# Kernel tuning notes

Measured on AMD Instinct MI355X. Metric: run time of the kernel, lower is better.

## Reference

```python
import jax, jax.numpy as jnp
import numpy as np

B, C, Cs, CI, H, W = 4, 256, 256, 128, 64, 64

def setup_inputs() -> dict:
    key = jax.random.key(0)
    ks = jax.random.split(key, 9)
    sq = 1.0 / np.sqrt(C)
    ss = 1.0 / np.sqrt(Cs)
    return {
        "x_main": jax.random.normal(ks[0], (B, C, H, W), jnp.float32),
        "z_p": jax.random.normal(ks[1], (B, Cs, H, W), jnp.float32),
        "Wq": jax.random.normal(ks[2], (CI, C), jnp.float32) * sq,
        "bq": jax.random.normal(ks[3], (CI,), jnp.float32) * 0.01,
        "Wk": jax.random.normal(ks[4], (CI, Cs), jnp.float32) * ss,
        "bk": jax.random.normal(ks[5], (CI,), jnp.float32) * 0.01,
        "Wv": jax.random.normal(ks[6], (C, Cs), jnp.float32) * ss,
        "bv": jax.random.normal(ks[7], (C,), jnp.float32) * 0.01,
        "gamma": jax.random.normal(ks[8], (1,), jnp.float32) * 0.1,
    }

def reference(x_main, z_p, Wq, bq, Wk, bk, Wv, bv, gamma):
    b, c, h, w = x_main.shape
    n = h * w
    xm = x_main.reshape(b, c, n)          # [B, C, N]
    zf = z_p.reshape(b, z_p.shape[1], n)  # [B, Cs, M] (M == N here)
    # 1x1 convs == per-pixel channel projections
    q = jnp.einsum('oc,bcn->bon', Wq, xm) + bq[None, :, None]  # [B, CI, N]
    k = jnp.einsum('oc,bcm->bom', Wk, zf) + bk[None, :, None]  # [B, CI, M]
    v = jnp.einsum('oc,bcm->bom', Wv, zf) + bv[None, :, None]  # [B, C, M]
    # energy[b, n, m] = q_n . k_m  (no scaling, as in the original)
    energy = jnp.einsum('bcn,bcm->bnm', q, k)
    attention = jax.nn.softmax(energy, axis=-1)
    out = jnp.einsum('bom,bnm->bon', v, attention)  # [B, C, N]
    out = out.reshape(b, c, h, w)
    return gamma * out + x_main
```

## Files before the change

kernel.cpp:

```cpp
#include <hip/hip_runtime.h>
#include <hip/hip_bf16.h>


typedef __bf16  bf16x8  __attribute__((ext_vector_type(8)));
typedef float   f32x16  __attribute__((ext_vector_type(16)));

#define LOG2E 1.4426950408889634f

union BF8 { __hip_bfloat162 h[4]; bf16x8 v; };
union U4  { unsigned u[4]; bf16x8 v; };

__device__ inline bf16x8 pack8(const float f[8]) {
  BF8 u;
#pragma unroll
  for (int i = 0; i < 4; i++)
    u.h[i] = __float22bfloat162_rn(float2{f[2 * i], f[2 * i + 1]});
  return u.v;
}

__device__ inline void dma16(const void* g, void* l) {
  __builtin_amdgcn_global_load_lds(
      (const __attribute__((address_space(1))) unsigned int*)g,
      (__attribute__((address_space(3))) unsigned int*)l, 16, 0, 0);
}

__global__ __launch_bounds__(256) void wprep_kernel(
    const float* __restrict__ Wq, const float* __restrict__ Wk,
    const float* __restrict__ Wv, __hip_bfloat16* __restrict__ wfr)
{
  const int base = blockIdx.x * 1024;
  const int tid = threadIdx.x;
#pragma unroll
  for (int i = 0; i < 4; i++) {
    int c = base + i * 256 + tid;
    const float* Ws; __hip_bfloat16* dst; int rc;
    if (c < 4096)      { Ws = Wq; dst = wfr;          rc = c; }
    else if (c < 8192) { Ws = Wk; dst = wfr + 32768;  rc = c - 4096; }
    else               { Ws = Wv; dst = wfr + 65536;  rc = c - 8192; }
    int ot = rc >> 10, cs = (rc >> 6) & 15, rem = rc & 63;
    int hf = rem >> 5, l32 = rem & 31;
    const float* src = Ws + (ot * 32 + l32) * 256 + cs * 16 + hf * 8;
    float f[8];
#pragma unroll
    for (int j = 0; j < 8; j++) f[j] = src[j];
    *(bf16x8*)(dst + ot * 8192 + cs * 512 + hf * 256 + l32 * 8) = pack8(f);
  }
}

struct PFSmem {
  float stg[128 * 68];
  alignas(16) __hip_bfloat16 frag[16384];
};

__global__ __launch_bounds__(512, 2) void projfused(
    const float* __restrict__ x, const float* __restrict__ z,
    const __hip_bfloat16* __restrict__ wfr,
    const float* __restrict__ bq, const float* __restrict__ bk,
    const float* __restrict__ bv,
    __hip_bfloat16* __restrict__ qp, __hip_bfloat16* __restrict__ kp,
    __hip_bfloat16* __restrict__ vp)
{
  __shared__ PFSmem sm;
  const int bi = blockIdx.x;
  const bool qmode = bi < 256;
  const int j2 = qmode ? bi : bi - 256;
  const int b = j2 >> 6, pc = j2 & 63;
  const float* in = qmode ? x : z;
  const size_t ib = (size_t)b * 256 * 4096 + pc * 64;

  const int tid = threadIdx.x, w = tid >> 6, lane = tid & 63,
            l32 = lane & 31, half = lane >> 5;
  const int pix4 = (tid & 15) * 4;

#pragma unroll
  for (int it = 0; it < 4; it++) {
    int ch = it * 32 + (tid >> 4);
    float4 v4 = *(const float4*)&in[ib + (size_t)ch * 4096 + pix4];
    *(float4*)&sm.stg[ch * 68 + pix4] = v4;
  }
  __syncthreads();
#pragma unroll
  for (int i = 0; i < 2; i++) {
    int c = i * 512 + tid;
    int grp = c >> 9, csl = (c >> 6) & 7, rem = c & 63;
    int hf = rem >> 5, lr = rem & 31;
    int chb = csl * 16 + hf * 8;
    float f[8];
#pragma unroll
    for (int j = 0; j < 8; j++) f[j] = sm.stg[(chb + j) * 68 + grp * 32 + lr];
    *(bf16x8*)(sm.frag + grp * 8192 + csl * 512 + hf * 256 + lr * 8) = pack8(f);
  }
  __syncthreads();

#pragma unroll
  for (int it = 0; it < 4; it++) {
    int ch = it * 32 + (tid >> 4);
    float4 v4 = *(const float4*)&in[ib + (size_t)(128 + ch) * 4096 + pix4];
    *(float4*)&sm.stg[ch * 68 + pix4] = v4;
  }
  __syncthreads();
#pragma unroll
  for (int i = 0; i < 2; i++) {
    int c = i * 512 + tid;
    int grp = c >> 9, csl = (c >> 6) & 7, rem = c & 63;
    int hf = rem >> 5, lr = rem & 31;
    int chb = csl * 16 + hf * 8;
    float f[8];
#pragma unroll
    for (int j = 0; j < 8; j++) f[j] = sm.stg[(chb + j) * 68 + grp * 32 + lr];
    *(bf16x8*)(sm.frag + grp * 8192 + (csl + 8) * 512 + hf * 256 + lr * 8) =
        pack8(f);
  }
  __syncthreads();

  const int t4 = (l32 >> 2) & 3;
  const int kperm = (t4 == 1 || t4 == 2) ? (l32 ^ 12) : l32;

  if (qmode) {
    const int ot = w >> 1, pg = w & 1;
    bf16x8 bfr[16];
#pragma unroll
    for (int cs = 0; cs < 16; cs++)
      bfr[cs] = *(const bf16x8*)(sm.frag + pg * 8192 + cs * 512 + lane * 8);
    const __hip_bfloat16* wp = wfr + ot * 8192 + lane * 8;
    bf16x8 wfg[16];
#pragma unroll
    for (int cs = 0; cs < 16; cs++) wfg[cs] = *(const bf16x8*)(wp + cs * 512);
    float bb[16];
#pragma unroll
    for (int r = 0; r < 16; r++)
      bb[r] = bq[ot * 32 + (r & 3) + 8 * (r >> 2) + 4 * half];
    f32x16 O = {};
#pragma unroll
    for (int cs = 0; cs < 16; cs++)
      O = __builtin_amdgcn_mfma_f32_32x32x16_bf16(wfg[cs], bfr[cs], O, 0, 0, 0);
    __hip_bfloat16* qb = qp + ((size_t)(b * 128 + pc * 2 + pg)) * 4096;
#pragma unroll
    for (int r = 0; r < 16; r++) {
      int oc = ot * 32 + (r & 3) + 8 * (r >> 2) + 4 * half;
      qb[(oc >> 4) * 512 + ((oc >> 3) & 1) * 256 + l32 * 8 + (oc & 7)] =
          __float2bfloat16((O[r] + bb[r]) * LOG2E);
    }
  } else {
    const int pg = w & 1;
    bf16x8 bfr[16];
#pragma unroll
    for (int cs = 0; cs < 16; cs++)
      bfr[cs] = *(const bf16x8*)(sm.frag + pg * 8192 + cs * 512 + lane * 8);
    const size_t pgg = (size_t)(b * 128 + pc * 2 + pg);
#pragma unroll
    for (int jj = 0; jj < 3; jj++) {
      const int t = (w + jj * 8) >> 1;
      const bool isK = (t < 4);
      const __hip_bfloat16* wp = wfr + (isK ? 32768 + t * 8192
                                            : 65536 + (t - 4) * 8192) + lane * 8;
      bf16x8 wfg[16];
#pragma unroll
      for (int cs = 0; cs < 16; cs++) wfg[cs] = *(const bf16x8*)(wp + cs * 512);
      const float* bias = isK ? bk : bv;
      const int ocb = (isK ? t : t - 4) * 32;
      float bb[16];
#pragma unroll
      for (int r = 0; r < 16; r++)
        bb[r] = bias[ocb + (r & 3) + 8 * (r >> 2) + 4 * half];
      f32x16 O = {};
#pragma unroll
      for (int cs = 0; cs < 16; cs++)
        O = __builtin_amdgcn_mfma_f32_32x32x16_bf16(wfg[cs], bfr[cs], O, 0, 0, 0);
      if (isK) {
        __hip_bfloat16* kb = kp + pgg * 4096;
#pragma unroll
        for (int r = 0; r < 16; r++) {
          int oc = t * 32 + (r & 3) + 8 * (r >> 2) + 4 * half;
          kb[(oc >> 4) * 512 + ((oc >> 3) & 1) * 256 + kperm * 8 + (oc & 7)] =
              __float2bfloat16(O[r] + bb[r]);
        }
      } else {
        __hip_bfloat16* vb = vp + pgg * 8192 + (t - 4) * 1024
            + (l32 >> 4) * 512 + ((l32 >> 3) & 1) * 256 + (l32 & 7);
#pragma unroll
        for (int r = 0; r < 16; r++) {
          int rr = (r & 3) + 8 * (r >> 2) + 4 * half;
          vb[rr * 8] = __float2bfloat16(O[r] + bb[r]);
        }
      }
    }
  }
}

struct AttnSmem {
  union {
    __hip_bfloat16 kbuf[3][8192];
    float ostage[256][33];
  } u;
  float redu[4][32];
  float rinv[32];
};

__global__ __launch_bounds__(256, 3) void attn_kernel(
    const __hip_bfloat16* __restrict__ qv, const __hip_bfloat16* __restrict__ kv,
    const __hip_bfloat16* __restrict__ vv,
    const float* __restrict__ x_main, const float* __restrict__ gammap,
    float* __restrict__ out)
{
  __shared__ AttnSmem sm;
  const int i  = blockIdx.x;
  const int b  = (i & 7) >> 1;
  const int qt = ((i >> 3) << 1) | (i & 1);
  const int n0 = qt * 32;
  const int tid  = threadIdx.x;
  const int w    = tid >> 6, lane = tid & 63, l32 = lane & 31;
  const int kh   = w >> 1, chh = w & 1;
  const int t0   = qt & 63;

  bf16x8 qf[8];
  {
    const __hip_bfloat16* qb = qv + ((size_t)(b * 128 + qt)) * 4096 + lane * 8;
#pragma unroll
    for (int cs = 0; cs < 8; cs++) qf[cs] = *(const bf16x8*)(qb + cs * 512);
  }

  const __hip_bfloat16* kg = kv + (size_t)(b * 128) * 4096;
  const __hip_bfloat16* vg = vv + (size_t)(b * 128) * 8192;

  auto stage = [&](int ta, int par) {
    __hip_bfloat16* kd = sm.u.kbuf[par];
    const __hip_bfloat16* ksrc = kg + (size_t)ta * 8192 + lane * 8;
#pragma unroll
    for (int c = 0; c < 4; c++) {
      int ck = w * 4 + c;
      dma16(ksrc + ck * 512, kd + ck * 512 + lane * 8);
    }
  };

  f32x16 Oacc[4];
#pragma unroll
  for (int c = 0; c < 4; c++)
#pragma unroll
    for (int r = 0; r < 16; r++) Oacc[c][r] = 0.f;

  float l_lane = 0.f;

  stage(t0, 0);
  stage((t0 + 1) & 63, 1);
  __syncthreads();

#pragma unroll 1
  for (int lt = 0; lt < 64; ++lt) {
    const int ta = (lt + t0) & 63;

    const __hip_bfloat16* vb = vg + (size_t)(ta * 2 + kh) * 8192
                             + chh * 4096 + lane * 8;
    bf16x8 Vc[8];
#pragma unroll
    for (int c = 0; c < 4; c++) {
      Vc[2 * c]     = *(const bf16x8*)(vb + c * 1024);
      Vc[2 * c + 1] = *(const bf16x8*)(vb + c * 1024 + 512);
    }
    __builtin_amdgcn_sched_barrier(0);

    if (lt < 62) stage((lt + 2 + t0) & 63, (lt + 2) % 3);

    const __hip_bfloat16* kbase = sm.u.kbuf[lt % 3] + kh * 4096 + lane * 8;
    f32x16 S = {};
#pragma unroll
    for (int cs = 0; cs < 8; cs++) {
      bf16x8 kf = *(const bf16x8*)(kbase + cs * 512);
      S = __builtin_amdgcn_mfma_f32_32x32x16_bf16(kf, qf[cs], S, 0, 0, 0);
    }

    unsigned p2[8];
    float lsub = 0.f;
#pragma unroll
    for (int i2 = 0; i2 < 8; i2++) {
      float a = exp2f(S[2 * i2]     - 64.0f);
      float c = exp2f(S[2 * i2 + 1] - 64.0f);
      lsub += a + c;
      union { __hip_bfloat162 h; unsigned u; } cv;
      cv.h = __float22bfloat162_rn(float2{a, c});
      p2[i2] = cv.u;
    }
    l_lane += lsub;
    U4 f0, f1;
    f0.u[0] = p2[0]; f0.u[1] = p2[1]; f0.u[2] = p2[2]; f0.u[3] = p2[3];
    f1.u[0] = p2[4]; f1.u[1] = p2[5]; f1.u[2] = p2[6]; f1.u[3] = p2[7];
    const bf16x8 pf0 = f0.v, pf1 = f1.v;

#pragma unroll
    for (int c = 0; c < 4; c++) {
      Oacc[c] = __builtin_amdgcn_mfma_f32_32x32x16_bf16(Vc[2 * c],     pf0, Oacc[c], 0, 0, 0);
      Oacc[c] = __builtin_amdgcn_mfma_f32_32x32x16_bf16(Vc[2 * c + 1], pf1, Oacc[c], 0, 0, 0);
    }

    if (lt < 63) {
      __builtin_amdgcn_sched_barrier(0);
      __builtin_amdgcn_s_barrier();
      __builtin_amdgcn_sched_barrier(0);
    }
  }

  float lfull = l_lane + __shfl_xor(l_lane, 32);
  if (lane < 32) sm.redu[w][l32] = lfull;
  __syncthreads();
  const int hb = lane >> 5;
  if (kh == 0) {
#pragma unroll
    for (int c = 0; c < 4; c++) {
#pragma unroll
      for (int r = 0; r < 16; r++) {
        int ch = (chh * 4 + c) * 32 + (r & 3) + 8 * (r >> 2) + 4 * hb;
        sm.u.ostage[ch][l32] = Oacc[c][r];
      }
    }
  }
  if (tid < 32) sm.rinv[tid] = 1.0f / (sm.redu[0][tid] + sm.redu[2][tid]);
  __syncthreads();
  if (kh == 1) {
#pragma unroll
    for (int c = 0; c < 4; c++) {
#pragma unroll
      for (int r = 0; r < 16; r++) {
        int ch = (chh * 4 + c) * 32 + (r & 3) + 8 * (r >> 2) + 4 * hb;
        sm.u.ostage[ch][l32] += Oacc[c][r];
      }
    }
  }
  __syncthreads();

  const float gmm = gammap[0];
  const int pix = tid & 31;
  const float ri = sm.rinv[pix];
#pragma unroll
  for (int j = 0; j < 32; ++j) {
    int ch = (tid >> 5) * 32 + j;
    size_t g = ((size_t)(b * 256 + ch)) * 4096 + n0 + pix;
    out[g] = gmm * sm.u.ostage[ch][pix] * ri + x_main[g];
  }
}

extern "C" void kernel_launch(void* const* d_in, const int* in_sizes, int n_in,
                              void* d_out, int out_size, void* d_ws, size_t ws_size,
                              hipStream_t stream) {
  (void)in_sizes; (void)n_in; (void)out_size; (void)ws_size;
  const float* x  = (const float*)d_in[0];
  const float* z  = (const float*)d_in[1];
  const float* Wq = (const float*)d_in[2];
  const float* bq = (const float*)d_in[3];
  const float* Wk = (const float*)d_in[4];
  const float* bk = (const float*)d_in[5];
  const float* Wv = (const float*)d_in[6];
  const float* bv = (const float*)d_in[7];
  const float* gm = (const float*)d_in[8];
  float* out = (float*)d_out;

  char* ws = (char*)d_ws;
  const size_t MB = 1024 * 1024;
  __hip_bfloat16* qp  = (__hip_bfloat16*)(ws);
  __hip_bfloat16* kp  = (__hip_bfloat16*)(ws + 4 * MB);
  __hip_bfloat16* vp  = (__hip_bfloat16*)(ws + 8 * MB);
  __hip_bfloat16* wfp = (__hip_bfloat16*)(ws + 16 * MB);

  wprep_kernel<<<16, 256, 0, stream>>>(Wq, Wk, Wv, wfp);
  projfused   <<<512, 512, 0, stream>>>(x, z, wfp, bq, bk, bv, qp, kp, vp);
  attn_kernel <<<512, 256, 0, stream>>>(qp, kp, vp, x, gm, out);
}
```

Measured before the change: 202.6 us.

## Process two query tiles per attention block to reuse K/V loads

Each attention block now handles 64 queries as two 32-query sub-tiles that share the same staged K tile and V registers, and the grid is halved to 256 blocks. Q moves into LDS, and the epilogue staging, row-sum reduction and output write are widened to 64 pixels. The aim is to halve global and LDS traffic for K and V per unit of work. In exchange, accumulator register use doubles and launch bounds drop to one block per CU, so fewer waves are left to hide latency.

```diff
diff --git a/kernel.cpp b/kernel.cpp
--- a/kernel.cpp
+++ b/kernel.cpp
@@ -190,41 +190,46 @@
 
 struct AttnSmem {
   union {
-    __hip_bfloat16 kbuf[3][8192];
-    float ostage[256][33];
+    struct {
+      __hip_bfloat16 kbuf[3][8192];
+      __hip_bfloat16 qlds[8192];
+    } m;
+    float ostage[256][65];
   } u;
-  float redu[4][32];
-  float rinv[32];
+  float redu[4][64];
+  float rinv[64];
 };
 
-__global__ __launch_bounds__(256, 3) void attn_kernel(
+__global__ __launch_bounds__(256, 1) void attn_kernel(
     const __hip_bfloat16* __restrict__ qv, const __hip_bfloat16* __restrict__ kv,
     const __hip_bfloat16* __restrict__ vv,
     const float* __restrict__ x_main, const float* __restrict__ gammap,
     float* __restrict__ out)
 {
   __shared__ AttnSmem sm;
-  const int i  = blockIdx.x;
-  const int b  = (i & 7) >> 1;
-  const int qt = ((i >> 3) << 1) | (i & 1);
-  const int n0 = qt * 32;
-  const int tid  = threadIdx.x;
-  const int w    = tid >> 6, lane = tid & 63, l32 = lane & 31;
-  const int kh   = w >> 1, chh = w & 1;
-  const int t0   = qt & 63;
-
-  bf16x8 qf[8];
+  const int i   = blockIdx.x;
+  const int b   = (i & 7) >> 1;
+  const int qt2 = ((i >> 3) << 1) | (i & 1);
+  const int qtA = qt2 * 2;
+  const int n0  = qt2 * 64;
+  const int tid = threadIdx.x;
+  const int w   = tid >> 6, lane = tid & 63, l32 = lane & 31;
+  const int kh  = w >> 1, chh = w & 1;
+  const int t0  = qt2 & 63;
+
   {
-    const __hip_bfloat16* qb = qv + ((size_t)(b * 128 + qt)) * 4096 + lane * 8;
-#pragma unroll
-    for (int cs = 0; cs < 8; cs++) qf[cs] = *(const bf16x8*)(qb + cs * 512);
+    const __hip_bfloat16* qsrc = qv + ((size_t)(b * 128 + qtA)) * 4096;
+#pragma unroll
+    for (int j = 0; j < 4; j++)
+      *(bf16x8*)(sm.u.m.qlds + j * 2048 + tid * 8) =
+          *(const bf16x8*)(qsrc + j * 2048 + tid * 8);
   }
 
   const __hip_bfloat16* kg = kv + (size_t)(b * 128) * 4096;
   const __hip_bfloat16* vg = vv + (size_t)(b * 128) * 8192;
 
   auto stage = [&](int ta, int par) {
-    __hip_bfloat16* kd = sm.u.kbuf[par];
+    __hip_bfloat16* kd = sm.u.m.kbuf[par];
     const __hip_bfloat16* ksrc = kg + (size_t)ta * 8192 + lane * 8;
 #pragma unroll
     for (int c = 0; c < 4; c++) {
@@ -233,42 +238,15 @@
     }
   };
 
-  f32x16 Oacc[4];
+  f32x16 OA[4], OB[4];
 #pragma unroll
   for (int c = 0; c < 4; c++)
 #pragma unroll
-    for (int r = 0; r < 16; r++) Oacc[c][r] = 0.f;
-
-  float l_lane = 0.f;
-
-  stage(t0, 0);
-  stage((t0 + 1) & 63, 1);
-  __syncthreads();
-
-#pragma unroll 1
-  for (int lt = 0; lt < 64; ++lt) {
-    const int ta = (lt + t0) & 63;
-
-    const __hip_bfloat16* vb = vg + (size_t)(ta * 2 + kh) * 8192
-                             + chh * 4096 + lane * 8;
-    bf16x8 Vc[8];
-#pragma unroll
-    for (int c = 0; c < 4; c++) {
-      Vc[2 * c]     = *(const bf16x8*)(vb + c * 1024);
-      Vc[2 * c + 1] = *(const bf16x8*)(vb + c * 1024 + 512);
-    }
-    __builtin_amdgcn_sched_barrier(0);
-
-    if (lt < 62) stage((lt + 2 + t0) & 63, (lt + 2) % 3);
-
-    const __hip_bfloat16* kbase = sm.u.kbuf[lt % 3] + kh * 4096 + lane * 8;
-    f32x16 S = {};
-#pragma unroll
-    for (int cs = 0; cs < 8; cs++) {
-      bf16x8 kf = *(const bf16x8*)(kbase + cs * 512);
-      S = __builtin_amdgcn_mfma_f32_32x32x16_bf16(kf, qf[cs], S, 0, 0, 0);
-    }
-
+    for (int r = 0; r < 16; r++) { OA[c][r] = 0.f; OB[c][r] = 0.f; }
+
+  float lA = 0.f, lB = 0.f;
+
+  auto softmax = [&](const f32x16& S, bf16x8& pf0, bf16x8& pf1, float& lacc) {
     unsigned p2[8];
     float lsub = 0.f;
 #pragma unroll
@@ -280,16 +258,57 @@
       cv.h = __float22bfloat162_rn(float2{a, c});
       p2[i2] = cv.u;
     }
-    l_lane += lsub;
+    lacc += lsub;
     U4 f0, f1;
     f0.u[0] = p2[0]; f0.u[1] = p2[1]; f0.u[2] = p2[2]; f0.u[3] = p2[3];
     f1.u[0] = p2[4]; f1.u[1] = p2[5]; f1.u[2] = p2[6]; f1.u[3] = p2[7];
-    const bf16x8 pf0 = f0.v, pf1 = f1.v;
-
-#pragma unroll
-    for (int c = 0; c < 4; c++) {
-      Oacc[c] = __builtin_amdgcn_mfma_f32_32x32x16_bf16(Vc[2 * c],     pf0, Oacc[c], 0, 0, 0);
-      Oacc[c] = __builtin_amdgcn_mfma_f32_32x32x16_bf16(Vc[2 * c + 1], pf1, Oacc[c], 0, 0, 0);
+    pf0 = f0.v; pf1 = f1.v;
+  };
+
+  stage(t0, 0);
+  stage((t0 + 1) & 63, 1);
+  __syncthreads();
+
+#pragma unroll 1
+  for (int lt = 0; lt < 64; ++lt) {
+    const int ta = (lt + t0) & 63;
+
+    const __hip_bfloat16* vb = vg + (size_t)(ta * 2 + kh) * 8192
+                             + chh * 4096 + lane * 8;
+    bf16x8 Vc[8];
+#pragma unroll
+    for (int c = 0; c < 4; c++) {
+      Vc[2 * c]     = *(const bf16x8*)(vb + c * 1024);
+      Vc[2 * c + 1] = *(const bf16x8*)(vb + c * 1024 + 512);
+    }
+    __builtin_amdgcn_sched_barrier(0);
+
+    if (lt < 62) stage((lt + 2 + t0) & 63, (lt + 2) % 3);
+
+    const __hip_bfloat16* kbase = sm.u.m.kbuf[lt % 3] + kh * 4096 + lane * 8;
+    const __hip_bfloat16* qab   = sm.u.m.qlds + lane * 8;
+    f32x16 SA = {}, SB = {};
+#pragma unroll
+    for (int cs = 0; cs < 8; cs++) {
+      bf16x8 kf = *(const bf16x8*)(kbase + cs * 512);
+      bf16x8 qa = *(const bf16x8*)(qab + cs * 512);
+      bf16x8 qb2 = *(const bf16x8*)(qab + 4096 + cs * 512);
+      SA = __builtin_amdgcn_mfma_f32_32x32x16_bf16(kf, qa,  SA, 0, 0, 0);
+      SB = __builtin_amdgcn_mfma_f32_32x32x16_bf16(kf, qb2, SB, 0, 0, 0);
+    }
+
+    bf16x8 pf0, pf1;
+    softmax(SA, pf0, pf1, lA);
+#pragma unroll
+    for (int c = 0; c < 4; c++) {
+      OA[c] = __builtin_amdgcn_mfma_f32_32x32x16_bf16(Vc[2 * c],     pf0, OA[c], 0, 0, 0);
+      OA[c] = __builtin_amdgcn_mfma_f32_32x32x16_bf16(Vc[2 * c + 1], pf1, OA[c], 0, 0, 0);
+    }
+    softmax(SB, pf0, pf1, lB);
+#pragma unroll
+    for (int c = 0; c < 4; c++) {
+      OB[c] = __builtin_amdgcn_mfma_f32_32x32x16_bf16(Vc[2 * c],     pf0, OB[c], 0, 0, 0);
+      OB[c] = __builtin_amdgcn_mfma_f32_32x32x16_bf16(Vc[2 * c + 1], pf1, OB[c], 0, 0, 0);
     }
 
     if (lt < 63) {
@@ -299,8 +318,9 @@
     }
   }
 
-  float lfull = l_lane + __shfl_xor(l_lane, 32);
-  if (lane < 32) sm.redu[w][l32] = lfull;
+  float lfA = lA + __shfl_xor(lA, 32);
+  float lfB = lB + __shfl_xor(lB, 32);
+  if (lane < 32) { sm.redu[w][l32] = lfA; sm.redu[w][32 + l32] = lfB; }
   __syncthreads();
   const int hb = lane >> 5;
   if (kh == 0) {
@@ -309,11 +329,12 @@
 #pragma unroll
       for (int r = 0; r < 16; r++) {
         int ch = (chh * 4 + c) * 32 + (r & 3) + 8 * (r >> 2) + 4 * hb;
-        sm.u.ostage[ch][l32] = Oacc[c][r];
+        sm.u.ostage[ch][l32]      = OA[c][r];
+        sm.u.ostage[ch][32 + l32] = OB[c][r];
       }
     }
   }
-  if (tid < 32) sm.rinv[tid] = 1.0f / (sm.redu[0][tid] + sm.redu[2][tid]);
+  if (tid < 64) sm.rinv[tid] = 1.0f / (sm.redu[0][tid] + sm.redu[2][tid]);
   __syncthreads();
   if (kh == 1) {
 #pragma unroll
@@ -321,18 +342,19 @@
 #pragma unroll
       for (int r = 0; r < 16; r++) {
         int ch = (chh * 4 + c) * 32 + (r & 3) + 8 * (r >> 2) + 4 * hb;
-        sm.u.ostage[ch][l32] += Oacc[c][r];
+        sm.u.ostage[ch][l32]      += OA[c][r];
+        sm.u.ostage[ch][32 + l32] += OB[c][r];
       }
     }
   }
   __syncthreads();
 
   const float gmm = gammap[0];
-  const int pix = tid & 31;
+  const int pix = tid & 63;
   const float ri = sm.rinv[pix];
-#pragma unroll
-  for (int j = 0; j < 32; ++j) {
-    int ch = (tid >> 5) * 32 + j;
+#pragma unroll 1
+  for (int j = 0; j < 64; ++j) {
+    int ch = j * 4 + (tid >> 6);
     size_t g = ((size_t)(b * 256 + ch)) * 4096 + n0 + pix;
     out[g] = gmm * sm.u.ostage[ch][pix] * ri + x_main[g];
   }
@@ -362,5 +384,5 @@
 
   wprep_kernel<<<16, 256, 0, stream>>>(Wq, Wk, Wv, wfp);
   projfused   <<<512, 512, 0, stream>>>(x, z, wfp, bq, bk, bv, qp, kp, vp);
-  attn_kernel <<<512, 256, 0, stream>>>(qp, kp, vp, x, gm, out);
-}
+  attn_kernel <<<256, 256, 0, stream>>>(qp, kp, vp, x, gm, out);
+}
```

New measurement: 227.3 us. +12.2%, slower.

## Split MFMA accumulation chains and stage Q/K projection outputs through LDS

Applied to the files above, without the earlier changes.

Splits each dependent MFMA accumulation chain into two independent accumulators (for the Q/K/V projections and the QK^T score product), so consecutive MFMAs do not wait on each other's results. In the projection kernel, Q and K outputs are first written into shared memory, then copied to global memory with coalesced 16-byte vector stores in place of scattered 2-byte stores. The cost is extra accumulator registers, an added barrier and LDS traffic, and slightly different floating-point summation order.

```diff
diff --git a/kernel.cpp b/kernel.cpp
--- a/kernel.cpp
+++ b/kernel.cpp
@@ -115,6 +115,7 @@
 
   const int t4 = (l32 >> 2) & 3;
   const int kperm = (t4 == 1 || t4 == 2) ? (l32 ^ 12) : l32;
+  __hip_bfloat16* ostg = (__hip_bfloat16*)sm.stg;
 
   if (qmode) {
     const int ot = w >> 1, pg = w & 1;
@@ -130,17 +131,23 @@
 #pragma unroll
     for (int r = 0; r < 16; r++)
       bb[r] = bq[ot * 32 + (r & 3) + 8 * (r >> 2) + 4 * half];
-    f32x16 O = {};
-#pragma unroll
-    for (int cs = 0; cs < 16; cs++)
-      O = __builtin_amdgcn_mfma_f32_32x32x16_bf16(wfg[cs], bfr[cs], O, 0, 0, 0);
-    __hip_bfloat16* qb = qp + ((size_t)(b * 128 + pc * 2 + pg)) * 4096;
+    f32x16 Oa = {}, Ob = {};
+#pragma unroll
+    for (int cs = 0; cs < 8; cs++) {
+      Oa = __builtin_amdgcn_mfma_f32_32x32x16_bf16(wfg[cs],     bfr[cs],     Oa, 0, 0, 0);
+      Ob = __builtin_amdgcn_mfma_f32_32x32x16_bf16(wfg[cs + 8], bfr[cs + 8], Ob, 0, 0, 0);
+    }
 #pragma unroll
     for (int r = 0; r < 16; r++) {
       int oc = ot * 32 + (r & 3) + 8 * (r >> 2) + 4 * half;
-      qb[(oc >> 4) * 512 + ((oc >> 3) & 1) * 256 + l32 * 8 + (oc & 7)] =
-          __float2bfloat16((O[r] + bb[r]) * LOG2E);
-    }
+      ostg[pg * 4096 + (oc >> 4) * 512 + ((oc >> 3) & 1) * 256 + l32 * 8 +
+           (oc & 7)] =
+          __float2bfloat16((Oa[r] + Ob[r] + bb[r]) * LOG2E);
+    }
+    __syncthreads();
+    __hip_bfloat16* qb = qp + ((size_t)(b * 128 + pc * 2)) * 4096;
+    *(bf16x8*)(qb + tid * 8)        = *(const bf16x8*)(ostg + tid * 8);
+    *(bf16x8*)(qb + 4096 + tid * 8) = *(const bf16x8*)(ostg + 4096 + tid * 8);
   } else {
     const int pg = w & 1;
     bf16x8 bfr[16];
@@ -148,41 +155,61 @@
     for (int cs = 0; cs < 16; cs++)
       bfr[cs] = *(const bf16x8*)(sm.frag + pg * 8192 + cs * 512 + lane * 8);
     const size_t pgg = (size_t)(b * 128 + pc * 2 + pg);
-#pragma unroll
-    for (int jj = 0; jj < 3; jj++) {
+
+    {
+      const int t = w >> 1;
+      const __hip_bfloat16* wp = wfr + 32768 + t * 8192 + lane * 8;
+      bf16x8 wfg[16];
+#pragma unroll
+      for (int cs = 0; cs < 16; cs++) wfg[cs] = *(const bf16x8*)(wp + cs * 512);
+      float bb[16];
+#pragma unroll
+      for (int r = 0; r < 16; r++)
+        bb[r] = bk[t * 32 + (r & 3) + 8 * (r >> 2) + 4 * half];
+      f32x16 Oa = {}, Ob = {};
+#pragma unroll
+      for (int cs = 0; cs < 8; cs++) {
+        Oa = __builtin_amdgcn_mfma_f32_32x32x16_bf16(wfg[cs],     bfr[cs],     Oa, 0, 0, 0);
+        Ob = __builtin_amdgcn_mfma_f32_32x32x16_bf16(wfg[cs + 8], bfr[cs + 8], Ob, 0, 0, 0);
+      }
+#pragma unroll
+      for (int r = 0; r < 16; r++) {
+        int oc = t * 32 + (r & 3) + 8 * (r >> 2) + 4 * half;
+        ostg[pg * 4096 + (oc >> 4) * 512 + ((oc >> 3) & 1) * 256 + kperm * 8 +
+             (oc & 7)] = __float2bfloat16(Oa[r] + Ob[r] + bb[r]);
+      }
+    }
+    __syncthreads();
+    {
+      __hip_bfloat16* kb = kp + ((size_t)(b * 128 + pc * 2)) * 4096;
+      *(bf16x8*)(kb + tid * 8)        = *(const bf16x8*)(ostg + tid * 8);
+      *(bf16x8*)(kb + 4096 + tid * 8) = *(const bf16x8*)(ostg + 4096 + tid * 8);
+    }
+
+#pragma unroll
+    for (int jj = 1; jj < 3; jj++) {
       const int t = (w + jj * 8) >> 1;
-      const bool isK = (t < 4);
-      const __hip_bfloat16* wp = wfr + (isK ? 32768 + t * 8192
-                                            : 65536 + (t - 4) * 8192) + lane * 8;
+      const int tt = t - 4;
+      const __hip_bfloat16* wp = wfr + 65536 + tt * 8192 + lane * 8;
       bf16x8 wfg[16];
 #pragma unroll
       for (int cs = 0; cs < 16; cs++) wfg[cs] = *(const bf16x8*)(wp + cs * 512);
-      const float* bias = isK ? bk : bv;
-      const int ocb = (isK ? t : t - 4) * 32;
       float bb[16];
 #pragma unroll
       for (int r = 0; r < 16; r++)
-        bb[r] = bias[ocb + (r & 3) + 8 * (r >> 2) + 4 * half];
-      f32x16 O = {};
-#pragma unroll
-      for (int cs = 0; cs < 16; cs++)
-        O = __builtin_amdgcn_mfma_f32_32x32x16_bf16(wfg[cs], bfr[cs], O, 0, 0, 0);
-      if (isK) {
-        __hip_bfloat16* kb = kp + pgg * 4096;
-#pragma unroll
-        for (int r = 0; r < 16; r++) {
-          int oc = t * 32 + (r & 3) + 8 * (r >> 2) + 4 * half;
-          kb[(oc >> 4) * 512 + ((oc >> 3) & 1) * 256 + kperm * 8 + (oc & 7)] =
-              __float2bfloat16(O[r] + bb[r]);
-        }
-      } else {
-        __hip_bfloat16* vb = vp + pgg * 8192 + (t - 4) * 1024
-            + (l32 >> 4) * 512 + ((l32 >> 3) & 1) * 256 + (l32 & 7);
-#pragma unroll
-        for (int r = 0; r < 16; r++) {
-          int rr = (r & 3) + 8 * (r >> 2) + 4 * half;
-          vb[rr * 8] = __float2bfloat16(O[r] + bb[r]);
-        }
+        bb[r] = bv[tt * 32 + (r & 3) + 8 * (r >> 2) + 4 * half];
+      f32x16 Oa = {}, Ob = {};
+#pragma unroll
+      for (int cs = 0; cs < 8; cs++) {
+        Oa = __builtin_amdgcn_mfma_f32_32x32x16_bf16(wfg[cs],     bfr[cs],     Oa, 0, 0, 0);
+        Ob = __builtin_amdgcn_mfma_f32_32x32x16_bf16(wfg[cs + 8], bfr[cs + 8], Ob, 0, 0, 0);
+      }
+      __hip_bfloat16* vb = vp + pgg * 8192 + tt * 1024
+          + (l32 >> 4) * 512 + ((l32 >> 3) & 1) * 256 + (l32 & 7);
+#pragma unroll
+      for (int r = 0; r < 16; r++) {
+        int rr = (r & 3) + 8 * (r >> 2) + 4 * half;
+        vb[rr * 8] = __float2bfloat16(Oa[r] + Ob[r] + bb[r]);
       }
     }
   }
@@ -262,19 +289,21 @@
     if (lt < 62) stage((lt + 2 + t0) & 63, (lt + 2) % 3);
 
     const __hip_bfloat16* kbase = sm.u.kbuf[lt % 3] + kh * 4096 + lane * 8;
-    f32x16 S = {};
-#pragma unroll
-    for (int cs = 0; cs < 8; cs++) {
-      bf16x8 kf = *(const bf16x8*)(kbase + cs * 512);
-      S = __builtin_amdgcn_mfma_f32_32x32x16_bf16(kf, qf[cs], S, 0, 0, 0);
+    f32x16 Sa = {}, Sb = {};
+#pragma unroll
+    for (int cs = 0; cs < 4; cs++) {
+      bf16x8 kfa = *(const bf16x8*)(kbase + cs * 512);
+      bf16x8 kfb = *(const bf16x8*)(kbase + (cs + 4) * 512);
+      Sa = __builtin_amdgcn_mfma_f32_32x32x16_bf16(kfa, qf[cs],     Sa, 0, 0, 0);
+      Sb = __builtin_amdgcn_mfma_f32_32x32x16_bf16(kfb, qf[cs + 4], Sb, 0, 0, 0);
     }
 
     unsigned p2[8];
     float lsub = 0.f;
 #pragma unroll
     for (int i2 = 0; i2 < 8; i2++) {
-      float a = exp2f(S[2 * i2]     - 64.0f);
-      float c = exp2f(S[2 * i2 + 1] - 64.0f);
+      float a = exp2f(Sa[2 * i2]     + Sb[2 * i2]     - 64.0f);
+      float c = exp2f(Sa[2 * i2 + 1] + Sb[2 * i2 + 1] - 64.0f);
       lsub += a + c;
       union { __hip_bfloat162 h; unsigned u; } cv;
       cv.h = __float22bfloat162_rn(float2{a, c});
```

Result: slower. 216.8 us (+7.0%).
